# Performance work log

Measured on AMD Instinct MI355X. Metric: run time of the kernel, lower is better.

The kernel has to match this reference:

```python
import jax, jax.numpy as jnp
import numpy as np

PAD, CLS, SEP, UNK = 0, 1, 2, 3
VOCAB, DIM, LATENT = 30000, 768, 5000
B, L, C = 16, 1024, 8


def setup_inputs() -> dict:
    key = jax.random.key(0)
    k1, k2, k3 = jax.random.split(key, 3)
    x = jax.random.randint(k1, (B, L, C), 0, VOCAB, dtype=jnp.int64)
    char_emb = jax.random.normal(k2, (VOCAB, DIM), dtype=jnp.float32)
    latent_mat = jax.random.normal(k3, (LATENT, DIM), dtype=jnp.float32) * (LATENT ** -0.5)
    return {"x": x, "char_emb": char_emb, "latent_mat": latent_mat}


def reference(x, char_emb, latent_mat):
    b, l, c = x.shape
    chars = x.reshape(-1, c)                       # (N, C)
    embs = char_emb[chars]                         # (N, C, D) gather
    pad_mask = chars == PAD                        # (N, C)
    embs = jnp.where(pad_mask[..., None], 0.0, embs)
    summed = embs.sum(axis=1)                      # (N, D)
    counts = jnp.clip((~pad_mask).sum(axis=-1), 1, None)  # (N,)
    lang_emb = jnp.tanh(summed / counts[:, None].astype(summed.dtype))  # (N, D)

    # soft codebook attention: matmul -> softmax -> matmul
    scores = jnp.einsum('nd,kd->nk', lang_emb, latent_mat)   # (N, LATENT)
    dist = jax.nn.softmax(scores, axis=-1)
    latent_emb = jnp.einsum('nk,kd->nd', dist, latent_mat)    # (N, D)
    sde = lang_emb + latent_emb

    # special-token overwrite based on first char id
    first = chars[:, 0]
    for tid in (PAD, UNK, SEP, CLS):
        sde = jnp.where((first == tid)[:, None], char_emb[tid], sde)
    return sde.reshape(b, l, -1)
```

## Files before the change

### kernel.cpp

```cpp
#include <hip/hip_runtime.h>

#define PAD_ID 0
#define NTOK   16384
#define DIM    768
#define KLAT   5000
#define KPAD   5024
#define NSTEP  157
#define TILE_SH 24576

typedef float f32x4 __attribute__((ext_vector_type(4)));
typedef __bf16 bf16x8 __attribute__((ext_vector_type(8)));

__device__ __forceinline__ unsigned short f2bf(float f) {
    unsigned int u = __float_as_uint(f);
    u += 0x7fffu + ((u >> 16) & 1u);
    return (unsigned short)(u >> 16);
}
__device__ __forceinline__ float bf2f(unsigned short h) {
    return __uint_as_float(((unsigned int)h) << 16);
}
__device__ __forceinline__ void async_cp16(const unsigned short* g, unsigned short* l) {
    __builtin_amdgcn_global_load_lds(
        (const __attribute__((address_space(1))) unsigned int*)g,
        (__attribute__((address_space(3))) unsigned int*)l, 16, 0, 0);
}

__global__ __launch_bounds__(256) void cvt_latS(const float* __restrict__ latent,
                                                unsigned short* __restrict__ latbS) {
    int g = blockIdx.x * 256 + threadIdx.x;
    if (g >= NSTEP * 24 * 2 * 64) return;
    int lane = g & 63; int rest = g >> 6;
    int h = rest & 1;  int kfr = rest >> 1;
    int kf = kfr % 24; int t  = kfr / 24;
    int row = t * 32 + h * 16 + (lane & 15);
    int col = kf * 32 + (lane >> 4) * 8;
    float4 v0 = make_float4(0.f,0.f,0.f,0.f), v1 = v0;
    if (row < KLAT) {
        v0 = *(const float4*)(latent + (long)row * DIM + col);
        v1 = *(const float4*)(latent + (long)row * DIM + col + 4);
    }
    uint4 o;
    o.x = (unsigned)f2bf(v0.x) | ((unsigned)f2bf(v0.y) << 16);
    o.y = (unsigned)f2bf(v0.z) | ((unsigned)f2bf(v0.w) << 16);
    o.z = (unsigned)f2bf(v1.x) | ((unsigned)f2bf(v1.y) << 16);
    o.w = (unsigned)f2bf(v1.z) | ((unsigned)f2bf(v1.w) << 16);
    *(uint4*)(latbS + (size_t)g * 8) = o;
}

__global__ __launch_bounds__(256) void cvt_latT(const float* __restrict__ latent,
                                                unsigned short* __restrict__ latbT) {
    int g = blockIdx.x * 256 + threadIdx.x;
    if (g >= NSTEP * DIM * 4) return;
    int kk8 = g & 3; int rest = g >> 2;
    int d = rest % DIM; int t = rest / DIM;
    int kk0 = kk8 * 8;
    unsigned short v[8];
    #pragma unroll
    for (int j = 0; j < 8; ++j) {
        int row = t * 32 + kk0 + j;
        v[j] = (row < KLAT) ? f2bf(latent[(long)row * DIM + d]) : (unsigned short)0;
    }
    *(uint4*)(latbT + (size_t)g * 8) = *(uint4*)v;
}

__global__ __launch_bounds__(192) void build_lang(const int* __restrict__ x,
                                                  const float* __restrict__ cemb,
                                                  unsigned short* __restrict__ langb) {
    int tok = blockIdx.x;
    int t = threadIdx.x;
    const int* xs = x + tok * 8;
    int ids[8]; int cnt = 0;
    #pragma unroll
    for (int c = 0; c < 8; ++c) { ids[c] = xs[c]; cnt += (ids[c] != PAD_ID); }
    float4 acc = make_float4(0.f, 0.f, 0.f, 0.f);
    #pragma unroll
    for (int c = 0; c < 8; ++c) {
        if (ids[c] != PAD_ID) {
            float4 v = *(const float4*)(cemb + (long)ids[c] * DIM + t * 4);
            acc.x += v.x; acc.y += v.y; acc.z += v.z; acc.w += v.w;
        }
    }
    float cntf = (float)max(cnt, 1);
    unsigned int u0 = (unsigned int)f2bf(tanhf(acc.x / cntf)) |
                      ((unsigned int)f2bf(tanhf(acc.y / cntf)) << 16);
    unsigned int u1 = (unsigned int)f2bf(tanhf(acc.z / cntf)) |
                      ((unsigned int)f2bf(tanhf(acc.w / cntf)) << 16);
    *(uint2*)(langb + tok * DIM + t * 4) = make_uint2(u0, u1);
}

__global__ __launch_bounds__(256, 1) void fused_sde(
        const int* __restrict__ x, const float* __restrict__ cemb,
        const unsigned short* __restrict__ langb,
        const unsigned short* __restrict__ latbS,
        const unsigned short* __restrict__ latbT,
        float* __restrict__ out) {
    __shared__ unsigned short sLat[TILE_SH];
    __shared__ unsigned short sP[64 * 40];
    __shared__ float sL[64];

    const int tid  = threadIdx.x;
    const int w    = tid >> 6;
    const int lane = tid & 63;
    const int ln   = lane & 15;
    const int quad = lane >> 4;
    const int m0   = blockIdx.x * 64;

    uint4 qf[24];
    {
        const unsigned short* qr = langb + (m0 + w * 16 + ln) * DIM;
        #pragma unroll
        for (int kf = 0; kf < 24; ++kf)
            qf[kf] = *(const uint4*)(qr + kf * 32 + quad * 8);
    }

    f32x4 accO[4][12];
    #pragma unroll
    for (int mt = 0; mt < 4; ++mt)
        #pragma unroll
        for (int dt = 0; dt < 12; ++dt)
            accO[mt][dt] = (f32x4){0.f, 0.f, 0.f, 0.f};
    float lpart = 0.f;

    #pragma unroll
    for (int i = 0; i < 12; ++i)
        async_cp16(latbS + ((size_t)i * 256 + tid) * 8,
                   sLat + (i * 256 + (tid & ~63)) * 8);
    __syncthreads();

    for (int s = 0; s < NSTEP; ++s) {
        uint4 bO[12];
        {
            const unsigned short* bt = latbT + (size_t)s * TILE_SH;
            #pragma unroll
            for (int dt = 0; dt < 12; ++dt)
                bO[dt] = *(const uint4*)(bt + (w * 192 + dt * 16 + ln) * 32 + quad * 8);
        }

        f32x4 s0 = {0.f,0.f,0.f,0.f}, s1 = {0.f,0.f,0.f,0.f};
        #pragma unroll
        for (int kf = 0; kf < 24; ++kf) {
            bf16x8 a0 = *(const bf16x8*)&sLat[(kf * 128 + lane) * 8];
            bf16x8 a1 = *(const bf16x8*)&sLat[(kf * 128 + 64 + lane) * 8];
            bf16x8 b  = *(const bf16x8*)&qf[kf];
            s0 = __builtin_amdgcn_mfma_f32_16x16x32_bf16(a0, b, s0, 0, 0, 0);
            s1 = __builtin_amdgcn_mfma_f32_16x16x32_bf16(a1, b, s1, 0, 0, 0);
        }

        {
            const int k0 = s * 32;
            unsigned short* prow = &sP[(w * 16 + ln) * 40];
            #pragma unroll
            for (int r = 0; r < 4; ++r) {
                int lat0 = k0 + quad * 4 + r;
                float e0 = (lat0 < KLAT) ? __expf(s0[r]) : 0.f;
                float e1 = (lat0 + 16 < KLAT) ? __expf(s1[r]) : 0.f;
                lpart += e0 + e1;
                prow[quad * 4 + r]      = f2bf(e0);
                prow[16 + quad * 4 + r] = f2bf(e1);
            }
        }
        __syncthreads();

        {
            int nt = (s + 1 < NSTEP) ? s + 1 : 0;
            const unsigned short* gs = latbS + (size_t)nt * TILE_SH;
            #pragma unroll
            for (int i = 0; i < 12; ++i)
                async_cp16(gs + (i * 256 + tid) * 8,
                           sLat + (i * 256 + (tid & ~63)) * 8);
        }

        bf16x8 pA[4];
        #pragma unroll
        for (int mt = 0; mt < 4; ++mt)
            pA[mt] = *(const bf16x8*)&sP[(mt * 16 + ln) * 40 + quad * 8];
        #pragma unroll
        for (int dt = 0; dt < 12; ++dt) {
            bf16x8 b = *(const bf16x8*)&bO[dt];
            #pragma unroll
            for (int mt = 0; mt < 4; ++mt)
                accO[mt][dt] = __builtin_amdgcn_mfma_f32_16x16x32_bf16(
                    pA[mt], b, accO[mt][dt], 0, 0, 0);
        }
        __syncthreads();
    }

    lpart += __shfl_xor(lpart, 16, 64);
    lpart += __shfl_xor(lpart, 32, 64);
    if (lane < 16) sL[w * 16 + lane] = lpart;
    __syncthreads();

    #pragma unroll
    for (int mt = 0; mt < 4; ++mt) {
        int tl0 = mt * 16 + quad * 4;
        float linv[4]; int fid[4];
        #pragma unroll
        for (int r = 0; r < 4; ++r) {
            linv[r] = 1.0f / sL[tl0 + r];
            fid[r]  = x[(m0 + tl0 + r) * 8];
        }
        #pragma unroll
        for (int dt = 0; dt < 12; ++dt) {
            int d = w * 192 + dt * 16 + ln;
            #pragma unroll
            for (int r = 0; r < 4; ++r) {
                int tok = m0 + tl0 + r;
                float v = accO[mt][dt][r] * linv[r] + bf2f(langb[tok * DIM + d]);
                if (fid[r] < 4) v = cemb[fid[r] * DIM + d];
                out[tok * DIM + d] = v;
            }
        }
    }
}

extern "C" void kernel_launch(void* const* d_in, const int* in_sizes, int n_in,
                              void* d_out, int out_size, void* d_ws, size_t ws_size,
                              hipStream_t stream) {
    const int*   x      = (const int*)d_in[0];
    const float* cemb   = (const float*)d_in[1];
    const float* latent = (const float*)d_in[2];
    float* out = (float*)d_out;

    unsigned short* langb = (unsigned short*)d_ws;
    unsigned short* latbS = langb + (size_t)NTOK * DIM;
    unsigned short* latbT = latbS + (size_t)NSTEP * TILE_SH;

    int nS = NSTEP * 24 * 2 * 64;
    int nT = NSTEP * DIM * 4;
    cvt_latS<<<(nS + 255) / 256, 256, 0, stream>>>(latent, latbS);
    cvt_latT<<<(nT + 255) / 256, 256, 0, stream>>>(latent, latbT);
    build_lang<<<NTOK, 192, 0, stream>>>(x, cemb, langb);
    fused_sde<<<NTOK / 64, 256, 0, stream>>>(x, cemb, langb, latbS, latbT, out);
}
```

Before: 582.2 us.

## Split score GEMM over K across wave pairs using 32x32x16 MFMA

The QK score stage switches from 16x16x32 to 32x32x16 MFMAs. Each wave computes a 32-token by 32-latent tile over half of the 768 feature dimension, and the two halves are reduced through shared memory before exp. This cuts the redundant per-wave LDS reads of the latent tile, adding an extra barrier and an LDS exchange in exchange. The two latent-conversion kernels are also merged into one launch, and tanhf is replaced by an exp-based fast tanh.

```diff
diff --git a/kernel.cpp b/kernel.cpp
--- a/kernel.cpp
+++ b/kernel.cpp
@@ -8,7 +8,8 @@
 #define NSTEP  157
 #define TILE_SH 24576
 
-typedef float f32x4 __attribute__((ext_vector_type(4)));
+typedef float f32x4  __attribute__((ext_vector_type(4)));
+typedef float f32x16 __attribute__((ext_vector_type(16)));
 typedef __bf16 bf16x8 __attribute__((ext_vector_type(8)));
 
 __device__ __forceinline__ unsigned short f2bf(float f) {
@@ -19,48 +20,48 @@
 __device__ __forceinline__ float bf2f(unsigned short h) {
     return __uint_as_float(((unsigned int)h) << 16);
 }
+__device__ __forceinline__ float fast_tanh(float x) {
+    return 1.0f - 2.0f / (__expf(2.0f * x) + 1.0f);
+}
 __device__ __forceinline__ void async_cp16(const unsigned short* g, unsigned short* l) {
     __builtin_amdgcn_global_load_lds(
         (const __attribute__((address_space(1))) unsigned int*)g,
         (__attribute__((address_space(3))) unsigned int*)l, 16, 0, 0);
 }
 
-__global__ __launch_bounds__(256) void cvt_latS(const float* __restrict__ latent,
-                                                unsigned short* __restrict__ latbS) {
+__global__ __launch_bounds__(256) void cvt_lat(const float* __restrict__ latent,
+                                               unsigned short* __restrict__ latbS,
+                                               unsigned short* __restrict__ latbT) {
     int g = blockIdx.x * 256 + threadIdx.x;
-    if (g >= NSTEP * 24 * 2 * 64) return;
-    int lane = g & 63; int rest = g >> 6;
-    int h = rest & 1;  int kfr = rest >> 1;
-    int kf = kfr % 24; int t  = kfr / 24;
-    int row = t * 32 + h * 16 + (lane & 15);
-    int col = kf * 32 + (lane >> 4) * 8;
-    float4 v0 = make_float4(0.f,0.f,0.f,0.f), v1 = v0;
-    if (row < KLAT) {
-        v0 = *(const float4*)(latent + (long)row * DIM + col);
-        v1 = *(const float4*)(latent + (long)row * DIM + col + 4);
-    }
-    uint4 o;
-    o.x = (unsigned)f2bf(v0.x) | ((unsigned)f2bf(v0.y) << 16);
-    o.y = (unsigned)f2bf(v0.z) | ((unsigned)f2bf(v0.w) << 16);
-    o.z = (unsigned)f2bf(v1.x) | ((unsigned)f2bf(v1.y) << 16);
-    o.w = (unsigned)f2bf(v1.z) | ((unsigned)f2bf(v1.w) << 16);
-    *(uint4*)(latbS + (size_t)g * 8) = o;
-}
-
-__global__ __launch_bounds__(256) void cvt_latT(const float* __restrict__ latent,
-                                                unsigned short* __restrict__ latbT) {
-    int g = blockIdx.x * 256 + threadIdx.x;
-    if (g >= NSTEP * DIM * 4) return;
-    int kk8 = g & 3; int rest = g >> 2;
-    int d = rest % DIM; int t = rest / DIM;
-    int kk0 = kk8 * 8;
-    unsigned short v[8];
-    #pragma unroll
-    for (int j = 0; j < 8; ++j) {
-        int row = t * 32 + kk0 + j;
-        v[j] = (row < KLAT) ? f2bf(latent[(long)row * DIM + d]) : (unsigned short)0;
-    }
-    *(uint4*)(latbT + (size_t)g * 8) = *(uint4*)v;
+    if (g >= NSTEP * 48 * 64) return;
+    {
+        int lane = g & 63; int rest = g >> 6;
+        int kf = rest % 48; int t = rest / 48;
+        int row = t * 32 + (lane & 31);
+        int col = kf * 16 + (lane >> 5) * 8;
+        float4 v0 = make_float4(0.f,0.f,0.f,0.f), v1 = v0;
+        if (row < KLAT) {
+            v0 = *(const float4*)(latent + (long)row * DIM + col);
+            v1 = *(const float4*)(latent + (long)row * DIM + col + 4);
+        }
+        uint4 o;
+        o.x = (unsigned)f2bf(v0.x) | ((unsigned)f2bf(v0.y) << 16);
+        o.y = (unsigned)f2bf(v0.z) | ((unsigned)f2bf(v0.w) << 16);
+        o.z = (unsigned)f2bf(v1.x) | ((unsigned)f2bf(v1.y) << 16);
+        o.w = (unsigned)f2bf(v1.z) | ((unsigned)f2bf(v1.w) << 16);
+        *(uint4*)(latbS + (size_t)g * 8) = o;
+    }
+    {
+        int kk8 = g & 3; int rest = g >> 2;
+        int d = rest % DIM; int t = rest / DIM;
+        unsigned short v[8];
+        #pragma unroll
+        for (int j = 0; j < 8; ++j) {
+            int row = t * 32 + kk8 * 8 + j;
+            v[j] = (row < KLAT) ? f2bf(latent[(long)row * DIM + d]) : (unsigned short)0;
+        }
+        *(uint4*)(latbT + (size_t)g * 8) = *(uint4*)v;
+    }
 }
 
 __global__ __launch_bounds__(192) void build_lang(const int* __restrict__ x,
@@ -80,11 +81,11 @@
             acc.x += v.x; acc.y += v.y; acc.z += v.z; acc.w += v.w;
         }
     }
-    float cntf = (float)max(cnt, 1);
-    unsigned int u0 = (unsigned int)f2bf(tanhf(acc.x / cntf)) |
-                      ((unsigned int)f2bf(tanhf(acc.y / cntf)) << 16);
-    unsigned int u1 = (unsigned int)f2bf(tanhf(acc.z / cntf)) |
-                      ((unsigned int)f2bf(tanhf(acc.w / cntf)) << 16);
+    float rc = 1.0f / (float)max(cnt, 1);
+    unsigned int u0 = (unsigned int)f2bf(fast_tanh(acc.x * rc)) |
+                      ((unsigned int)f2bf(fast_tanh(acc.y * rc)) << 16);
+    unsigned int u1 = (unsigned int)f2bf(fast_tanh(acc.z * rc)) |
+                      ((unsigned int)f2bf(fast_tanh(acc.w * rc)) << 16);
     *(uint2*)(langb + tok * DIM + t * 4) = make_uint2(u0, u1);
 }
 
@@ -95,22 +96,28 @@
         const unsigned short* __restrict__ latbT,
         float* __restrict__ out) {
     __shared__ unsigned short sLat[TILE_SH];
-    __shared__ unsigned short sP[64 * 40];
-    __shared__ float sL[64];
+    __shared__ float4 sX[2][4][64];
+    __shared__ unsigned short sP[64 * 44];
+    __shared__ float sLh[2][64];
 
     const int tid  = threadIdx.x;
     const int w    = tid >> 6;
     const int lane = tid & 63;
-    const int ln   = lane & 15;
-    const int quad = lane >> 4;
+    const int h    = w & 1;
+    const int t    = w >> 1;
+    const int ln31 = lane & 31;
+    const int hb   = lane >> 5;
+    const int ln16 = lane & 15;
+    const int q4   = lane >> 4;
     const int m0   = blockIdx.x * 64;
 
     uint4 qf[24];
     {
-        const unsigned short* qr = langb + (m0 + w * 16 + ln) * DIM;
-        #pragma unroll
-        for (int kf = 0; kf < 24; ++kf)
-            qf[kf] = *(const uint4*)(qr + kf * 32 + quad * 8);
+        const unsigned short* qr = langb + (size_t)(m0 + t * 32 + ln31) * DIM
+                                   + h * 384 + hb * 8;
+        #pragma unroll
+        for (int i = 0; i < 24; ++i)
+            qf[i] = *(const uint4*)(qr + i * 16);
     }
 
     f32x4 accO[4][12];
@@ -133,31 +140,25 @@
             const unsigned short* bt = latbT + (size_t)s * TILE_SH;
             #pragma unroll
             for (int dt = 0; dt < 12; ++dt)
-                bO[dt] = *(const uint4*)(bt + (w * 192 + dt * 16 + ln) * 32 + quad * 8);
-        }
-
-        f32x4 s0 = {0.f,0.f,0.f,0.f}, s1 = {0.f,0.f,0.f,0.f};
-        #pragma unroll
-        for (int kf = 0; kf < 24; ++kf) {
-            bf16x8 a0 = *(const bf16x8*)&sLat[(kf * 128 + lane) * 8];
-            bf16x8 a1 = *(const bf16x8*)&sLat[(kf * 128 + 64 + lane) * 8];
-            bf16x8 b  = *(const bf16x8*)&qf[kf];
-            s0 = __builtin_amdgcn_mfma_f32_16x16x32_bf16(a0, b, s0, 0, 0, 0);
-            s1 = __builtin_amdgcn_mfma_f32_16x16x32_bf16(a1, b, s1, 0, 0, 0);
-        }
-
-        {
-            const int k0 = s * 32;
-            unsigned short* prow = &sP[(w * 16 + ln) * 40];
-            #pragma unroll
-            for (int r = 0; r < 4; ++r) {
-                int lat0 = k0 + quad * 4 + r;
-                float e0 = (lat0 < KLAT) ? __expf(s0[r]) : 0.f;
-                float e1 = (lat0 + 16 < KLAT) ? __expf(s1[r]) : 0.f;
-                lpart += e0 + e1;
-                prow[quad * 4 + r]      = f2bf(e0);
-                prow[16 + quad * 4 + r] = f2bf(e1);
-            }
+                bO[dt] = *(const uint4*)(bt + (w * 192 + dt * 16 + ln16) * 32 + q4 * 8);
+        }
+
+        f32x16 De, Do;
+        #pragma unroll
+        for (int i2 = 0; i2 < 16; ++i2) { De[i2] = 0.f; Do[i2] = 0.f; }
+        #pragma unroll
+        for (int i = 0; i < 24; ++i) {
+            bf16x8 a = *(const bf16x8*)&sLat[((h * 24 + i) * 64 + lane) * 8];
+            bf16x8 b = *(const bf16x8*)&qf[i];
+            if (i & 1) Do = __builtin_amdgcn_mfma_f32_32x32x16_bf16(a, b, Do, 0, 0, 0);
+            else       De = __builtin_amdgcn_mfma_f32_32x32x16_bf16(a, b, De, 0, 0, 0);
+        }
+        f32x16 D = De + Do;
+
+        #pragma unroll
+        for (int g2 = 0; g2 < 2; ++g2) {
+            int rb = ((1 - h) * 2 + g2) * 4;
+            sX[g2][w][lane] = make_float4(D[rb], D[rb + 1], D[rb + 2], D[rb + 3]);
         }
         __syncthreads();
 
@@ -170,10 +171,32 @@
                            sLat + (i * 256 + (tid & ~63)) * 8);
         }
 
+        #pragma unroll
+        for (int g2 = 0; g2 < 2; ++g2) {
+            float4 p = sX[g2][w ^ 1][lane];
+            int rb = (h * 2 + g2) * 4;
+            float v0 = D[rb]     + p.x;
+            float v1 = D[rb + 1] + p.y;
+            float v2 = D[rb + 2] + p.z;
+            float v3 = D[rb + 3] + p.w;
+            int row0 = (2 * h + g2) * 8 + 4 * hb;
+            int base = s * 32 + row0;
+            float e0 = (base     < KLAT) ? __expf(v0) : 0.f;
+            float e1 = (base + 1 < KLAT) ? __expf(v1) : 0.f;
+            float e2 = (base + 2 < KLAT) ? __expf(v2) : 0.f;
+            float e3 = (base + 3 < KLAT) ? __expf(v3) : 0.f;
+            lpart += (e0 + e1) + (e2 + e3);
+            uint2 pk;
+            pk.x = (unsigned)f2bf(e0) | ((unsigned)f2bf(e1) << 16);
+            pk.y = (unsigned)f2bf(e2) | ((unsigned)f2bf(e3) << 16);
+            *(uint2*)&sP[(t * 32 + ln31) * 44 + row0] = pk;
+        }
+        __syncthreads();
+
         bf16x8 pA[4];
         #pragma unroll
         for (int mt = 0; mt < 4; ++mt)
-            pA[mt] = *(const bf16x8*)&sP[(mt * 16 + ln) * 40 + quad * 8];
+            pA[mt] = *(const bf16x8*)&sP[(mt * 16 + ln16) * 44 + q4 * 8];
         #pragma unroll
         for (int dt = 0; dt < 12; ++dt) {
             bf16x8 b = *(const bf16x8*)&bO[dt];
@@ -185,29 +208,28 @@
         __syncthreads();
     }
 
-    lpart += __shfl_xor(lpart, 16, 64);
     lpart += __shfl_xor(lpart, 32, 64);
-    if (lane < 16) sL[w * 16 + lane] = lpart;
+    if (lane < 32) sLh[h][t * 32 + lane] = lpart;
     __syncthreads();
 
     #pragma unroll
     for (int mt = 0; mt < 4; ++mt) {
-        int tl0 = mt * 16 + quad * 4;
+        int tl0 = mt * 16 + q4 * 4;
         float linv[4]; int fid[4];
         #pragma unroll
         for (int r = 0; r < 4; ++r) {
-            linv[r] = 1.0f / sL[tl0 + r];
+            linv[r] = 1.0f / (sLh[0][tl0 + r] + sLh[1][tl0 + r]);
             fid[r]  = x[(m0 + tl0 + r) * 8];
         }
         #pragma unroll
         for (int dt = 0; dt < 12; ++dt) {
-            int d = w * 192 + dt * 16 + ln;
+            int d = w * 192 + dt * 16 + ln16;
             #pragma unroll
             for (int r = 0; r < 4; ++r) {
                 int tok = m0 + tl0 + r;
-                float v = accO[mt][dt][r] * linv[r] + bf2f(langb[tok * DIM + d]);
-                if (fid[r] < 4) v = cemb[fid[r] * DIM + d];
-                out[tok * DIM + d] = v;
+                float v = accO[mt][dt][r] * linv[r] + bf2f(langb[(size_t)tok * DIM + d]);
+                if (fid[r] < 4) v = cemb[(size_t)fid[r] * DIM + d];
+                out[(size_t)tok * DIM + d] = v;
             }
         }
     }
@@ -225,10 +247,8 @@
     unsigned short* latbS = langb + (size_t)NTOK * DIM;
     unsigned short* latbT = latbS + (size_t)NSTEP * TILE_SH;
 
-    int nS = NSTEP * 24 * 2 * 64;
-    int nT = NSTEP * DIM * 4;
-    cvt_latS<<<(nS + 255) / 256, 256, 0, stream>>>(latent, latbS);
-    cvt_latT<<<(nT + 255) / 256, 256, 0, stream>>>(latent, latbT);
+    int nG = NSTEP * 48 * 64;
+    cvt_lat<<<(nG + 255) / 256, 256, 0, stream>>>(latent, latbS, latbT);
     build_lang<<<NTOK, 192, 0, stream>>>(x, cemb, langb);
     fused_sde<<<NTOK / 64, 256, 0, stream>>>(x, cemb, langb, latbS, latbT, out);
 }
```

Result: slower. 694.9 us (+19.3%).
